# Performance work log

Measured on AMD Instinct MI355X. Metric: run time of the kernel, lower is better.

The kernel has to match this reference:

```python
import jax, jax.numpy as jnp
import numpy as np

N_NODES = 50000
N_EDGES = 800000
HEADS = 4
HID = 48
NEG_SLOPE = 0.2


def setup_inputs() -> dict:
    key = jax.random.key(0)
    ks = list(jax.random.split(key, 32))
    inp = {}
    inp['x'] = jax.random.normal(ks[0], (N_NODES, 3), dtype=jnp.float32)
    inp['edge_index'] = jax.random.randint(ks[1], (2, N_EDGES), 0, N_NODES, dtype=jnp.int64)
    dims = [3, HID, HID]
    ki = 2
    for li, din in enumerate(dims):
        s = 1.0 / np.sqrt(din)
        inp[f'Wl{li}'] = jax.random.normal(ks[ki], (din, HEADS * HID), dtype=jnp.float32) * s; ki += 1
        inp[f'bl{li}'] = jnp.zeros((HEADS * HID,), dtype=jnp.float32)
        inp[f'Wr{li}'] = jax.random.normal(ks[ki], (din, HEADS * HID), dtype=jnp.float32) * s; ki += 1
        inp[f'br{li}'] = jnp.zeros((HEADS * HID,), dtype=jnp.float32)
        inp[f'att{li}'] = jax.random.normal(ks[ki], (HEADS, HID), dtype=jnp.float32) * (1.0 / np.sqrt(HID)); ki += 1
        inp[f'bias{li}'] = jnp.zeros((HID,), dtype=jnp.float32)
    inp['head_w'] = jax.random.normal(ks[ki], (HID, 1), dtype=jnp.float32) * (1.0 / np.sqrt(HID))
    inp['head_b'] = jnp.full((1,), 0.1, dtype=jnp.float32)
    return inp


def _gatv2_layer(x, src, dst, Wl, bl, Wr, br, att, bias):
    # GATv2Conv, concat=False, eval mode (dropout off), self-loops already in (src,dst)
    N = x.shape[0]
    xl = (x @ Wl + bl).reshape(N, HEADS, HID)  # source transform
    xr = (x @ Wr + br).reshape(N, HEADS, HID)  # target transform
    e = jax.nn.leaky_relu(xl[src] + xr[dst], NEG_SLOPE)  # [E,H,C]
    score = jnp.einsum('ehc,hc->eh', e, att)             # [E,H]
    # segment softmax over edges grouped by destination node
    m = jax.ops.segment_max(score, dst, num_segments=N)
    p = jnp.exp(score - m[dst])
    denom = jax.ops.segment_sum(p, dst, num_segments=N)
    alpha = p / (denom[dst] + 1e-16)                     # [E,H]
    out = jax.ops.segment_sum(alpha[..., None] * xl[src], dst, num_segments=N)  # [N,H,C]
    return out.mean(axis=1) + bias  # concat=False -> mean over heads


def reference(x, edge_index, Wl0, bl0, Wr0, br0, att0, bias0,
              Wl1, bl1, Wr1, br1, att1, bias1,
              Wl2, bl2, Wr2, br2, att2, bias2, head_w, head_b):
    N = x.shape[0]
    loops = jnp.arange(N, dtype=edge_index.dtype)
    src = jnp.concatenate([edge_index[0], loops])  # PyG add_self_loops=True
    dst = jnp.concatenate([edge_index[1], loops])
    params = [(Wl0, bl0, Wr0, br0, att0, bias0),
              (Wl1, bl1, Wr1, br1, att1, bias1),
              (Wl2, bl2, Wr2, br2, att2, bias2)]
    for (Wl, bl, Wr, br, att, bias) in params:
        x = _gatv2_layer(x, src, dst, Wl, bl, Wr, br, att, bias)
        x = jax.nn.elu(x)
    out = (x @ head_w + head_b)[:, 0]
    return jax.nn.relu(out)
```

## Files before the change

kernel.cpp:

```cpp
#include <hip/hip_runtime.h>
#include <hip/hip_bf16.h>
#include <math.h>

#define HEADS 4
#define HID 48
#define FDIM 192
#define NEG_SLOPE 0.2f

typedef float f4 __attribute__((ext_vector_type(4)));

template<int CTRL>
__device__ __forceinline__ float dpp_add(float v) {
    int t = __builtin_amdgcn_update_dpp(0, __float_as_int(v), CTRL, 0xF, 0xF, true);
    return v + __int_as_float(t);
}
__device__ __forceinline__ float red16(float v) {
    v = dpp_add<0xB1>(v);
    v = dpp_add<0x4E>(v);
    v = dpp_add<0x124>(v);
    v = dpp_add<0x128>(v);
    return v;
}

__global__ void detect_kernel(const int* __restrict__ ei, int* __restrict__ flag) {
    int l = (int)threadIdx.x;
    int v = ei[2 * l + 1];
    unsigned long long b = __ballot(v != 0);
    if (l == 0) *flag = (b == 0ULL) ? 1 : 0;
}

__global__ void hist_kernel(const int* __restrict__ ei, const int* __restrict__ flag,
                            int* __restrict__ deg, int E, int E2) {
    int is64 = *flag;
    for (int e = blockIdx.x * blockDim.x + threadIdx.x; e < E2;
         e += gridDim.x * blockDim.x) {
        int d;
        if (e < E) d = is64 ? ei[2 * (E + e)] : ei[E + e];
        else       d = e - E;
        atomicAdd(&deg[d], 1);
    }
}

__global__ void scan_local_kernel(const int* __restrict__ deg, int* __restrict__ incl,
                                  int* __restrict__ bsum, int N) {
    __shared__ int sm[256];
    int i = blockIdx.x * 256 + threadIdx.x;
    int v = (i < N) ? deg[i] : 0;
    sm[threadIdx.x] = v;
    __syncthreads();
    #pragma unroll
    for (int off = 1; off < 256; off <<= 1) {
        int t = ((int)threadIdx.x >= off) ? sm[threadIdx.x - off] : 0;
        __syncthreads();
        sm[threadIdx.x] += t;
        __syncthreads();
    }
    if (i < N) incl[i] = sm[threadIdx.x];
    if (threadIdx.x == 255) bsum[blockIdx.x] = sm[255];
}

__global__ void scan_bsum_kernel(int* __restrict__ bsum, int nb) {
    __shared__ int sm[256];
    __shared__ int running;
    if (threadIdx.x == 0) running = 0;
    __syncthreads();
    for (int base = 0; base < nb; base += 256) {
        int i = base + (int)threadIdx.x;
        int v = (i < nb) ? bsum[i] : 0;
        sm[threadIdx.x] = v;
        __syncthreads();
        #pragma unroll
        for (int off = 1; off < 256; off <<= 1) {
            int t = ((int)threadIdx.x >= off) ? sm[threadIdx.x - off] : 0;
            __syncthreads();
            sm[threadIdx.x] += t;
            __syncthreads();
        }
        if (i < nb) bsum[i] = running + sm[threadIdx.x] - v;
        __syncthreads();
        if (threadIdx.x == 0) running += sm[255];
        __syncthreads();
    }
}

__global__ void scan_final_kernel(const int* __restrict__ incl, const int* __restrict__ bsum,
                                  int* __restrict__ rowptr, int N) {
    int i = blockIdx.x * 256 + threadIdx.x;
    if (i < N) rowptr[i + 1] = incl[i] + bsum[blockIdx.x];
    if (i == 0) rowptr[0] = 0;
}

__global__ void scatter_kernel(const int* __restrict__ ei, const int* __restrict__ flag,
                               const int* __restrict__ rowptr, int* __restrict__ cursor,
                               int* __restrict__ srcs, int E, int E2) {
    int is64 = *flag;
    for (int e = blockIdx.x * blockDim.x + threadIdx.x; e < E2;
         e += gridDim.x * blockDim.x) {
        int s, d;
        if (e < E) {
            if (is64) { s = ei[2 * e]; d = ei[2 * (E + e)]; }
            else      { s = ei[e];     d = ei[E + e]; }
        } else {
            s = d = e - E;
        }
        int pos = rowptr[d] + atomicAdd(&cursor[d], 1);
        srcs[pos] = s;
    }
}

template<int DIN>
__global__ __launch_bounds__(192) void gemm2t_kernel(
    const float* __restrict__ xin,
    const float* __restrict__ Wl, const float* __restrict__ bl,
    const float* __restrict__ Wr, const float* __restrict__ br,
    float* __restrict__ xl, float* __restrict__ xr, int N) {
    int t  = (int)threadIdx.x;
    int cg = t % 48;
    int ng = t / 48;
    int c0 = cg * 4;
    int n0 = blockIdx.x * 16 + ng * 4;
    if (n0 >= N) return;

    f4 bLv = *(const f4*)&bl[c0];
    f4 bRv = *(const f4*)&br[c0];
    f4 accL[4], accR[4];
    #pragma unroll
    for (int i = 0; i < 4; ++i) { accL[i] = bLv; accR[i] = bRv; }

    if (n0 + 3 < N) {
        if (DIN == 3) {
            float xv[4][3];
            #pragma unroll
            for (int i = 0; i < 4; ++i) {
                const float* xp = xin + (size_t)(n0 + i) * 3;
                xv[i][0] = xp[0]; xv[i][1] = xp[1]; xv[i][2] = xp[2];
            }
            #pragma unroll
            for (int k = 0; k < 3; ++k) {
                f4 wl4 = *(const f4*)&Wl[k * FDIM + c0];
                f4 wr4 = *(const f4*)&Wr[k * FDIM + c0];
                #pragma unroll
                for (int i = 0; i < 4; ++i) {
                    float xs = xv[i][k];
                    accL[i] += xs * wl4;
                    accR[i] += xs * wr4;
                }
            }
        } else {
            #pragma unroll
            for (int kk = 0; kk < DIN; kk += 8) {
                float xv[4][8];
                #pragma unroll
                for (int i = 0; i < 4; ++i) {
                    const float* xp = xin + (size_t)(n0 + i) * DIN + kk;
                    f4 xa = *(const f4*)xp;
                    f4 xb = *(const f4*)(xp + 4);
                    #pragma unroll
                    for (int q = 0; q < 4; ++q) { xv[i][q] = xa[q]; xv[i][4 + q] = xb[q]; }
                }
                #pragma unroll
                for (int k = 0; k < 8; ++k) {
                    f4 wl4 = *(const f4*)&Wl[(kk + k) * FDIM + c0];
                    f4 wr4 = *(const f4*)&Wr[(kk + k) * FDIM + c0];
                    #pragma unroll
                    for (int i = 0; i < 4; ++i) {
                        float xs = xv[i][k];
                        accL[i] += xs * wl4;
                        accR[i] += xs * wr4;
                    }
                }
            }
        }
        #pragma unroll
        for (int i = 0; i < 4; ++i) {
            *(f4*)&xl[(size_t)(n0 + i) * FDIM + c0] = accL[i];
            *(f4*)&xr[(size_t)(n0 + i) * FDIM + c0] = accR[i];
        }
    } else {
        for (int i = 0; i < 4; ++i) {
            int n = n0 + i;
            if (n >= N) break;
            f4 aL = bLv;
            f4 aR = bRv;
            for (int k = 0; k < DIN; ++k) {
                float xs = xin[(size_t)n * DIN + k];
                f4 wl4 = *(const f4*)&Wl[k * FDIM + c0];
                f4 wr4 = *(const f4*)&Wr[k * FDIM + c0];
                aL += xs * wl4;
                aR += xs * wr4;
            }
            *(f4*)&xl[(size_t)n * FDIM + c0] = aL;
            *(f4*)&xr[(size_t)n * FDIM + c0] = aR;
        }
    }
}

__global__ __launch_bounds__(256) void gat_layer_kernel(
    const float* __restrict__ xl, const float* __restrict__ xr,
    const float* __restrict__ att, const float* __restrict__ bias,
    const int* __restrict__ rowptr, const int* __restrict__ srcs,
    float* __restrict__ xout,
    float* __restrict__ out,
    const float* __restrict__ head_w, const float* __restrict__ head_b,
    int N, int final_flag) {
    int wave = (int)((blockIdx.x * blockDim.x + threadIdx.x) >> 6);
    int lane = (int)(threadIdx.x & 63);
    if (wave >= N) return;
    int n  = wave;
    int h  = lane >> 4;
    int cl = lane & 15;
    int j0 = h * HID + cl;

    float a0 = att[j0], a1 = att[j0 + 16], a2 = att[j0 + 32];
    const float* xrp = xr + (size_t)n * FDIM;
    float r0 = xrp[j0], r1 = xrp[j0 + 16], r2 = xrp[j0 + 32];

    float m = -INFINITY, denom = 0.f;
    float acc0 = 0.f, acc1 = 0.f, acc2 = 0.f;

    int e0 = rowptr[n], e1 = rowptr[n + 1];
    int e = e0;
    for (; e + 1 < e1; e += 2) {
        int sa = srcs[e], sb = srcs[e + 1];
        const float* xa = xl + (size_t)sa * FDIM;
        const float* xb = xl + (size_t)sb * FDIM;
        float al0 = xa[j0], al1 = xa[j0 + 16], al2 = xa[j0 + 32];
        float bl0 = xb[j0], bl1 = xb[j0 + 16], bl2 = xb[j0 + 32];

        float ta0 = al0 + r0; ta0 = (ta0 > 0.f) ? ta0 : NEG_SLOPE * ta0;
        float ta1 = al1 + r1; ta1 = (ta1 > 0.f) ? ta1 : NEG_SLOPE * ta1;
        float ta2 = al2 + r2; ta2 = (ta2 > 0.f) ? ta2 : NEG_SLOPE * ta2;
        float tb0 = bl0 + r0; tb0 = (tb0 > 0.f) ? tb0 : NEG_SLOPE * tb0;
        float tb1 = bl1 + r1; tb1 = (tb1 > 0.f) ? tb1 : NEG_SLOPE * tb1;
        float tb2 = bl2 + r2; tb2 = (tb2 > 0.f) ? tb2 : NEG_SLOPE * tb2;
        float sA = red16(ta0 * a0 + ta1 * a1 + ta2 * a2);
        float sB = red16(tb0 * a0 + tb1 * a1 + tb2 * a2);

        float nm    = fmaxf(m, fmaxf(sA, sB));
        float scale = __expf(m - nm);
        float pa    = __expf(sA - nm);
        float pb    = __expf(sB - nm);
        denom = denom * scale + pa + pb;
        acc0  = acc0 * scale + pa * al0 + pb * bl0;
        acc1  = acc1 * scale + pa * al1 + pb * bl1;
        acc2  = acc2 * scale + pa * al2 + pb * bl2;
        m = nm;
    }
    if (e < e1) {
        int s = srcs[e];
        const float* xa = xl + (size_t)s * FDIM;
        float l0 = xa[j0], l1 = xa[j0 + 16], l2 = xa[j0 + 32];
        float t0 = l0 + r0; t0 = (t0 > 0.f) ? t0 : NEG_SLOPE * t0;
        float t1 = l1 + r1; t1 = (t1 > 0.f) ? t1 : NEG_SLOPE * t1;
        float t2 = l2 + r2; t2 = (t2 > 0.f) ? t2 : NEG_SLOPE * t2;
        float sA = red16(t0 * a0 + t1 * a1 + t2 * a2);
        float nm    = fmaxf(m, sA);
        float scale = __expf(m - nm);
        float p     = __expf(sA - nm);
        denom = denom * scale + p;
        acc0  = acc0 * scale + p * l0;
        acc1  = acc1 * scale + p * l1;
        acc2  = acc2 * scale + p * l2;
        m = nm;
    }

    float inv = 1.0f / (denom + 1e-16f);
    float o0 = acc0 * inv, o1 = acc1 * inv, o2 = acc2 * inv;
    o0 += __shfl_xor(o0, 16); o0 += __shfl_xor(o0, 32);
    o1 += __shfl_xor(o1, 16); o1 += __shfl_xor(o1, 32);
    o2 += __shfl_xor(o2, 16); o2 += __shfl_xor(o2, 32);
    o0 = 0.25f * o0 + bias[cl];
    o1 = 0.25f * o1 + bias[cl + 16];
    o2 = 0.25f * o2 + bias[cl + 32];
    o0 = (o0 > 0.f) ? o0 : expm1f(o0);
    o1 = (o1 > 0.f) ? o1 : expm1f(o1);
    o2 = (o2 > 0.f) ? o2 : expm1f(o2);

    if (!final_flag) {
        if (h == 0) {
            float* xo = xout + (size_t)n * HID;
            xo[cl] = o0; xo[cl + 16] = o1; xo[cl + 32] = o2;
        }
    } else {
        float part = o0 * head_w[cl] + o1 * head_w[cl + 16] + o2 * head_w[cl + 32];
        part = red16(part);
        if (lane == 0) {
            float v = part + head_b[0];
            out[n] = (v > 0.f) ? v : 0.f;
        }
    }
}

extern "C" void kernel_launch(void* const* d_in, const int* in_sizes, int n_in,
                              void* d_out, int out_size, void* d_ws, size_t ws_size,
                              hipStream_t stream) {
    const float* x0 = (const float*)d_in[0];
    const int*   ei = (const int*)d_in[1];

    const int N  = in_sizes[0] / 3;
    const int E  = in_sizes[1] / 2;
    const int E2 = E + N;

    const float* Wl[3];  const float* bl[3];
    const float* Wr[3];  const float* br[3];
    const float* att[3]; const float* bias[3];
    for (int li = 0; li < 3; ++li) {
        int b = 2 + 6 * li;
        Wl[li]   = (const float*)d_in[b + 0];
        bl[li]   = (const float*)d_in[b + 1];
        Wr[li]   = (const float*)d_in[b + 2];
        br[li]   = (const float*)d_in[b + 3];
        att[li]  = (const float*)d_in[b + 4];
        bias[li] = (const float*)d_in[b + 5];
    }
    const float* head_w = (const float*)d_in[20];
    const float* head_b = (const float*)d_in[21];
    float* out = (float*)d_out;

    size_t off = 0;
    auto alloc = [&](size_t bytes) -> void* {
        void* p = (char*)d_ws + off;
        off = (off + bytes + 255) & ~(size_t)255;
        return p;
    };
    const int nb = (N + 255) / 256;
    int*   flag   = (int*)alloc(sizeof(int));
    int*   deg    = (int*)alloc((size_t)N * sizeof(int));
    int*   incl   = (int*)alloc((size_t)N * sizeof(int));
    int*   bsum   = (int*)alloc((size_t)nb * sizeof(int));
    int*   rowptr = (int*)alloc((size_t)(N + 1) * sizeof(int));
    int*   srcs   = (int*)alloc((size_t)E2 * sizeof(int));
    float* xlb    = (float*)alloc((size_t)N * FDIM * sizeof(float));
    float* xrb    = (float*)alloc((size_t)N * FDIM * sizeof(float));
    float* xbuf   = (float*)alloc((size_t)N * HID * sizeof(float));
    (void)ws_size;

    detect_kernel<<<1, 64, 0, stream>>>(ei, flag);
    (void)hipMemsetAsync(deg, 0, (size_t)N * sizeof(int), stream);
    hist_kernel<<<2048, 256, 0, stream>>>(ei, flag, deg, E, E2);
    scan_local_kernel<<<nb, 256, 0, stream>>>(deg, incl, bsum, N);
    scan_bsum_kernel<<<1, 256, 0, stream>>>(bsum, nb);
    scan_final_kernel<<<nb, 256, 0, stream>>>(incl, bsum, rowptr, N);
    (void)hipMemsetAsync(deg, 0, (size_t)N * sizeof(int), stream);
    scatter_kernel<<<2048, 256, 0, stream>>>(ei, flag, rowptr, deg, srcs, E, E2);

    const int waves_per_block = 4;
    int gat_blocks = (N + waves_per_block - 1) / waves_per_block;
    int gemm_blocks = (N + 15) / 16;

    gemm2t_kernel<3><<<gemm_blocks, 192, 0, stream>>>(x0, Wl[0], bl[0], Wr[0], br[0], xlb, xrb, N);
    gat_layer_kernel<<<gat_blocks, 256, 0, stream>>>(xlb, xrb, att[0], bias[0],
        rowptr, srcs, xbuf, nullptr, nullptr, nullptr, N, 0);

    gemm2t_kernel<HID><<<gemm_blocks, 192, 0, stream>>>(xbuf, Wl[1], bl[1], Wr[1], br[1], xlb, xrb, N);
    gat_layer_kernel<<<gat_blocks, 256, 0, stream>>>(xlb, xrb, att[1], bias[1],
        rowptr, srcs, xbuf, nullptr, nullptr, nullptr, N, 0);

    gemm2t_kernel<HID><<<gemm_blocks, 192, 0, stream>>>(xbuf, Wl[2], bl[2], Wr[2], br[2], xlb, xrb, N);
    gat_layer_kernel<<<gat_blocks, 256, 0, stream>>>(xlb, xrb, att[2], bias[2],
        rowptr, srcs, nullptr, out, head_w, head_b, N, 1);

    (void)n_in; (void)out_size;
}
```

Baseline: 497.2 us.

## Unroll GAT aggregation by four with deferred softmax rescaling and fold setup launches

The GAT edge loop now processes four edges per iteration with clamped indices and masked scores, issuing more independent gathers per wave. Online-softmax rescaling is skipped unless some score exceeds the running max by a threshold, which removes most rescale exponentials. Separately, the int64-detection kernel is inlined into the histogram and scatter kernels, and the cursor reset is folded into the scan-final kernel, dropping one launch and one memset. The deferred rescaling lets exponentials grow up to e^8 relative to the running max, which slightly changes numerical behaviour. The masked tail lanes also do redundant loads.

```diff
diff --git a/kernel.cpp b/kernel.cpp
--- a/kernel.cpp
+++ b/kernel.cpp
@@ -22,16 +22,15 @@
     return v;
 }
 
-__global__ void detect_kernel(const int* __restrict__ ei, int* __restrict__ flag) {
-    int l = (int)threadIdx.x;
+__device__ __forceinline__ int detect64(const int* __restrict__ ei) {
+    int l = (int)(threadIdx.x & 63);
     int v = ei[2 * l + 1];
-    unsigned long long b = __ballot(v != 0);
-    if (l == 0) *flag = (b == 0ULL) ? 1 : 0;
-}
-
-__global__ void hist_kernel(const int* __restrict__ ei, const int* __restrict__ flag,
+    return (__ballot(v != 0) == 0ULL) ? 1 : 0;
+}
+
+__global__ void hist_kernel(const int* __restrict__ ei,
                             int* __restrict__ deg, int E, int E2) {
-    int is64 = *flag;
+    int is64 = detect64(ei);
     for (int e = blockIdx.x * blockDim.x + threadIdx.x; e < E2;
          e += gridDim.x * blockDim.x) {
         int d;
@@ -84,16 +83,16 @@
 }
 
 __global__ void scan_final_kernel(const int* __restrict__ incl, const int* __restrict__ bsum,
-                                  int* __restrict__ rowptr, int N) {
+                                  int* __restrict__ rowptr, int* __restrict__ cursor, int N) {
     int i = blockIdx.x * 256 + threadIdx.x;
-    if (i < N) rowptr[i + 1] = incl[i] + bsum[blockIdx.x];
+    if (i < N) { rowptr[i + 1] = incl[i] + bsum[blockIdx.x]; cursor[i] = 0; }
     if (i == 0) rowptr[0] = 0;
 }
 
-__global__ void scatter_kernel(const int* __restrict__ ei, const int* __restrict__ flag,
+__global__ void scatter_kernel(const int* __restrict__ ei,
                                const int* __restrict__ rowptr, int* __restrict__ cursor,
                                int* __restrict__ srcs, int E, int E2) {
-    int is64 = *flag;
+    int is64 = detect64(ei);
     for (int e = blockIdx.x * blockDim.x + threadIdx.x; e < E2;
          e += gridDim.x * blockDim.x) {
         int s, d;
@@ -195,6 +194,10 @@
     }
 }
 
+#define SCORE_MASKED (-1e38f)
+#define M_INIT       (-3e38f)
+#define DEFER_THR    8.0f
+
 __global__ __launch_bounds__(256) void gat_layer_kernel(
     const float* __restrict__ xl, const float* __restrict__ xr,
     const float* __restrict__ att, const float* __restrict__ bias,
@@ -204,8 +207,9 @@
     const float* __restrict__ head_w, const float* __restrict__ head_b,
     int N, int final_flag) {
     int wave = (int)((blockIdx.x * blockDim.x + threadIdx.x) >> 6);
+    wave = __builtin_amdgcn_readfirstlane(wave);
+    if (wave >= N) return;
     int lane = (int)(threadIdx.x & 63);
-    if (wave >= N) return;
     int n  = wave;
     int h  = lane >> 4;
     int cl = lane & 15;
@@ -215,53 +219,55 @@
     const float* xrp = xr + (size_t)n * FDIM;
     float r0 = xrp[j0], r1 = xrp[j0 + 16], r2 = xrp[j0 + 32];
 
-    float m = -INFINITY, denom = 0.f;
+    float m = M_INIT, denom = 0.f;
     float acc0 = 0.f, acc1 = 0.f, acc2 = 0.f;
 
     int e0 = rowptr[n], e1 = rowptr[n + 1];
-    int e = e0;
-    for (; e + 1 < e1; e += 2) {
-        int sa = srcs[e], sb = srcs[e + 1];
-        const float* xa = xl + (size_t)sa * FDIM;
-        const float* xb = xl + (size_t)sb * FDIM;
-        float al0 = xa[j0], al1 = xa[j0 + 16], al2 = xa[j0 + 32];
-        float bl0 = xb[j0], bl1 = xb[j0 + 16], bl2 = xb[j0 + 32];
-
-        float ta0 = al0 + r0; ta0 = (ta0 > 0.f) ? ta0 : NEG_SLOPE * ta0;
-        float ta1 = al1 + r1; ta1 = (ta1 > 0.f) ? ta1 : NEG_SLOPE * ta1;
-        float ta2 = al2 + r2; ta2 = (ta2 > 0.f) ? ta2 : NEG_SLOPE * ta2;
-        float tb0 = bl0 + r0; tb0 = (tb0 > 0.f) ? tb0 : NEG_SLOPE * tb0;
-        float tb1 = bl1 + r1; tb1 = (tb1 > 0.f) ? tb1 : NEG_SLOPE * tb1;
-        float tb2 = bl2 + r2; tb2 = (tb2 > 0.f) ? tb2 : NEG_SLOPE * tb2;
-        float sA = red16(ta0 * a0 + ta1 * a1 + ta2 * a2);
-        float sB = red16(tb0 * a0 + tb1 * a1 + tb2 * a2);
-
-        float nm    = fmaxf(m, fmaxf(sA, sB));
-        float scale = __expf(m - nm);
-        float pa    = __expf(sA - nm);
-        float pb    = __expf(sB - nm);
-        denom = denom * scale + pa + pb;
-        acc0  = acc0 * scale + pa * al0 + pb * bl0;
-        acc1  = acc1 * scale + pa * al1 + pb * bl1;
-        acc2  = acc2 * scale + pa * al2 + pb * bl2;
-        m = nm;
-    }
-    if (e < e1) {
-        int s = srcs[e];
-        const float* xa = xl + (size_t)s * FDIM;
-        float l0 = xa[j0], l1 = xa[j0 + 16], l2 = xa[j0 + 32];
-        float t0 = l0 + r0; t0 = (t0 > 0.f) ? t0 : NEG_SLOPE * t0;
-        float t1 = l1 + r1; t1 = (t1 > 0.f) ? t1 : NEG_SLOPE * t1;
-        float t2 = l2 + r2; t2 = (t2 > 0.f) ? t2 : NEG_SLOPE * t2;
-        float sA = red16(t0 * a0 + t1 * a1 + t2 * a2);
-        float nm    = fmaxf(m, sA);
-        float scale = __expf(m - nm);
-        float p     = __expf(sA - nm);
-        denom = denom * scale + p;
-        acc0  = acc0 * scale + p * l0;
-        acc1  = acc1 * scale + p * l1;
-        acc2  = acc2 * scale + p * l2;
-        m = nm;
+    int elast = e1 - 1;
+
+    for (int e = e0; e < e1; e += 4) {
+        int i0 = e,     i1 = e + 1,  i2 = e + 2,  i3 = e + 3;
+        int k0 = (i0 < e1) ? i0 : elast;
+        int k1 = (i1 < e1) ? i1 : elast;
+        int k2 = (i2 < e1) ? i2 : elast;
+        int k3 = (i3 < e1) ? i3 : elast;
+        int s0 = srcs[k0], s1 = srcs[k1], s2 = srcs[k2], s3 = srcs[k3];
+        const float* p0 = xl + (size_t)s0 * FDIM;
+        const float* p1 = xl + (size_t)s1 * FDIM;
+        const float* p2 = xl + (size_t)s2 * FDIM;
+        const float* p3 = xl + (size_t)s3 * FDIM;
+        float l00 = p0[j0], l01 = p0[j0 + 16], l02 = p0[j0 + 32];
+        float l10 = p1[j0], l11 = p1[j0 + 16], l12 = p1[j0 + 32];
+        float l20 = p2[j0], l21 = p2[j0 + 16], l22 = p2[j0 + 32];
+        float l30 = p3[j0], l31 = p3[j0 + 16], l32 = p3[j0 + 32];
+
+        #define LRELU(x) (fmaf(NEG_SLOPE, fminf((x), 0.f), fmaxf((x), 0.f)))
+        float sc0 = LRELU(l00 + r0) * a0 + LRELU(l01 + r1) * a1 + LRELU(l02 + r2) * a2;
+        float sc1 = LRELU(l10 + r0) * a0 + LRELU(l11 + r1) * a1 + LRELU(l12 + r2) * a2;
+        float sc2 = LRELU(l20 + r0) * a0 + LRELU(l21 + r1) * a1 + LRELU(l22 + r2) * a2;
+        float sc3 = LRELU(l30 + r0) * a0 + LRELU(l31 + r1) * a1 + LRELU(l32 + r2) * a2;
+        #undef LRELU
+        sc0 = red16(sc0); sc1 = red16(sc1); sc2 = red16(sc2); sc3 = red16(sc3);
+        sc0 = (i0 < e1) ? sc0 : SCORE_MASKED;
+        sc1 = (i1 < e1) ? sc1 : SCORE_MASKED;
+        sc2 = (i2 < e1) ? sc2 : SCORE_MASKED;
+        sc3 = (i3 < e1) ? sc3 : SCORE_MASKED;
+
+        float bmax = fmaxf(fmaxf(sc0, sc1), fmaxf(sc2, sc3));
+        if (__any(bmax > m + DEFER_THR)) {
+            float nm = fmaxf(m, bmax);
+            float sc = __expf(m - nm);
+            denom *= sc; acc0 *= sc; acc1 *= sc; acc2 *= sc;
+            m = nm;
+        }
+        float q0 = __expf(sc0 - m);
+        float q1 = __expf(sc1 - m);
+        float q2 = __expf(sc2 - m);
+        float q3 = __expf(sc3 - m);
+        denom += (q0 + q1) + (q2 + q3);
+        acc0 = fmaf(q0, l00, fmaf(q1, l10, fmaf(q2, l20, fmaf(q3, l30, acc0))));
+        acc1 = fmaf(q0, l01, fmaf(q1, l11, fmaf(q2, l21, fmaf(q3, l31, acc1))));
+        acc2 = fmaf(q0, l02, fmaf(q1, l12, fmaf(q2, l22, fmaf(q3, l32, acc2))));
     }
 
     float inv = 1.0f / (denom + 1e-16f);
@@ -324,7 +330,6 @@
         return p;
     };
     const int nb = (N + 255) / 256;
-    int*   flag   = (int*)alloc(sizeof(int));
     int*   deg    = (int*)alloc((size_t)N * sizeof(int));
     int*   incl   = (int*)alloc((size_t)N * sizeof(int));
     int*   bsum   = (int*)alloc((size_t)nb * sizeof(int));
@@ -335,14 +340,12 @@
     float* xbuf   = (float*)alloc((size_t)N * HID * sizeof(float));
     (void)ws_size;
 
-    detect_kernel<<<1, 64, 0, stream>>>(ei, flag);
     (void)hipMemsetAsync(deg, 0, (size_t)N * sizeof(int), stream);
-    hist_kernel<<<2048, 256, 0, stream>>>(ei, flag, deg, E, E2);
+    hist_kernel<<<2048, 256, 0, stream>>>(ei, deg, E, E2);
     scan_local_kernel<<<nb, 256, 0, stream>>>(deg, incl, bsum, N);
     scan_bsum_kernel<<<1, 256, 0, stream>>>(bsum, nb);
-    scan_final_kernel<<<nb, 256, 0, stream>>>(incl, bsum, rowptr, N);
-    (void)hipMemsetAsync(deg, 0, (size_t)N * sizeof(int), stream);
-    scatter_kernel<<<2048, 256, 0, stream>>>(ei, flag, rowptr, deg, srcs, E, E2);
+    scan_final_kernel<<<nb, 256, 0, stream>>>(incl, bsum, rowptr, deg, N);
+    scatter_kernel<<<2048, 256, 0, stream>>>(ei, rowptr, deg, srcs, E, E2);
 
     const int waves_per_block = 4;
     int gat_blocks = (N + waves_per_block - 1) / waves_per_block;
```

Measured after the change: 480.0 us. 1.04x faster.
